# Kernel optimization log

Hardware: AMD Instinct MI355X
Metric: run time of the kernel (lower is better)

## Reference

```python
import jax, jax.numpy as jnp
import numpy as np

B, F, L, T, U, A, CF = 512, 80, 111, 222, 20, 10, 32  # batch, feat, enc_len, dec_steps, lstm units, attn units, conv filters


def setup_inputs() -> dict:
    key = jax.random.key(0)
    ks = jax.random.split(key, 16)
    g = lambda i, shape: jax.random.normal(ks[i], shape, jnp.float32) * 0.2
    return {
        "inputs": jax.random.normal(ks[0], (B, L, F), jnp.float32),
        "enc_Wx": g(1, (F, 4 * U)), "enc_Wh": g(2, (U, 4 * U)), "enc_b": jnp.zeros((4 * U,), jnp.float32),
        "att_Wq": g(3, (U, A)), "att_bq": jnp.zeros((A,), jnp.float32),
        "att_Wm": g(4, (U, A)), "att_bm": jnp.zeros((A,), jnp.float32),
        "att_V": g(5, (A, 1)), "att_bv": jnp.zeros((1,), jnp.float32),
        "loc_Wconv": g(6, (1, CF)),  # Conv1D kernel_size=1, no bias -> matmul
        "loc_Wd": g(7, (CF, A)),
        "dec_Wx": g(8, (U, 4 * U)), "dec_Wh": g(9, (U, 4 * U)), "dec_b": jnp.zeros((4 * U,), jnp.float32),
        "out_W": g(10, (U, 1)), "out_b": jnp.zeros((1,), jnp.float32),
    }


def _lstm(z, h, c):
    # Keras LSTMCell gate order: i, f, g(cell), o
    i, f, g, o = jnp.split(z, 4, axis=-1)
    c_new = jax.nn.sigmoid(f) * c + jax.nn.sigmoid(i) * jnp.tanh(g)
    h_new = jax.nn.sigmoid(o) * jnpp_tanh(c_new) if False else jax.nn.sigmoid(o) * jnp.tanh(c_new)
    return h_new, c_new


def reference(inputs, enc_Wx, enc_Wh, enc_b, att_Wq, att_bq, att_Wm, att_bm,
              att_V, att_bv, loc_Wconv, loc_Wd, dec_Wx, dec_Wh, dec_b, out_W, out_b):
    Bb, Ll = inputs.shape[0], inputs.shape[1]
    h0 = jnp.zeros((Bb, U), inputs.dtype)
    c0 = jnp.zeros((Bb, U), inputs.dtype)

    # ---- encoder LSTM(20), return_sequences ----
    def enc_step(carry, x_t):
        h, c = carry
        h, c = _lstm(x_t @ enc_Wx + h @ enc_Wh + enc_b, h, c)
        return (h, c), h
    _, enc_seq = jax.lax.scan(enc_step, (h0, c0), jnp.swapaxes(inputs, 0, 1))
    enc_out = jnp.swapaxes(enc_seq, 0, 1)                 # [B, L, U]
    mem_proj = enc_out @ att_Wm + att_bm                  # hoisted memory projection [B, L, A]

    # ---- decoder: location-sensitive attention + LSTMCell per step ----
    def dec_step(carry, _):
        h, c, prev_attn = carry                           # prev_attn: [B, L, 1]
        # Source unpacks Keras states as (c, h) but Keras order is [h, c]:
        # the query is actually the LSTM cell state. Replicated faithfully.
        q = c @ att_Wq + att_bq                           # [B, A]
        loc = jnp.tanh((prev_attn @ loc_Wconv) @ loc_Wd)  # kernel_size=1 conv == matmul, [B, L, A]
        score = jnp.tanh(mem_proj + q[:, None, :] + loc) @ att_V + att_bv  # [B, L, 1]
        attn = jax.nn.softmax(score, axis=1)              # softmax over encoder length
        ctx = jnp.sum(attn * enc_out, axis=1)             # [B, U]
        h_new, c_new = _lstm(ctx @ dec_Wx + h @ dec_Wh + dec_b, h, c)
        y = jnp.tanh(h_new @ out_W + out_b)               # [B, 1]
        return (h_new, c_new, attn), y

    a0 = jnp.zeros((Bb, Ll, 1), inputs.dtype)
    _, ys = jax.lax.scan(dec_step, (h0, c0, a0), None, length=T)
    return jnp.swapaxes(ys, 0, 1)                         # [B, T, 1] == output[:, :, :-length]
```

## Files before the change

kernel.cpp:

```cpp
#include <hip/hip_runtime.h>
#include <math.h>

#define NB    512
#define FDIM  80
#define LEN   111
#define TDEC  222
#define CFDIM 32
#define EOS   113

typedef float v2 __attribute__((ext_vector_type(2)));

__device__ __forceinline__ float rcpf(float x){ return __builtin_amdgcn_rcpf(x); }
__device__ __forceinline__ float sigm(float x){ return rcpf(1.0f + __expf(-x)); }
__device__ __forceinline__ float ftanh(float x){
  float e = __expf(2.0f*x);
  return 1.0f - 2.0f*rcpf(e + 1.0f);
}

template<int CTRL, int ROW_MASK>
__device__ __forceinline__ float dpp_add(float x){
  int yi = __builtin_amdgcn_update_dpp(0, __builtin_bit_cast(int, x), CTRL, ROW_MASK, 0xf, false);
  return x + __builtin_bit_cast(float, yi);
}
__device__ __forceinline__ float wave_sum(float x){
  x = dpp_add<0x111, 0xf>(x);
  x = dpp_add<0x112, 0xf>(x);
  x = dpp_add<0x114, 0xf>(x);
  x = dpp_add<0x118, 0xf>(x);
  x = dpp_add<0x142, 0xa>(x);
  x = dpp_add<0x143, 0xc>(x);
  return __builtin_bit_cast(float, __builtin_amdgcn_readlane(__builtin_bit_cast(int, x), 63));
}
#define RL(x, u) __builtin_bit_cast(float, __builtin_amdgcn_readlane(__builtin_bit_cast(int, (x)), (u)))

__global__ __launch_bounds__(64, 1)
void attn_rnn_kernel(const float* __restrict__ g_in,
                     const float* __restrict__ enc_Wx, const float* __restrict__ enc_Wh, const float* __restrict__ enc_b,
                     const float* __restrict__ att_Wq, const float* __restrict__ att_bq,
                     const float* __restrict__ att_Wm, const float* __restrict__ att_bm,
                     const float* __restrict__ att_V,  const float* __restrict__ att_bv,
                     const float* __restrict__ loc_Wc, const float* __restrict__ loc_Wd,
                     const float* __restrict__ dec_Wx, const float* __restrict__ dec_Wh, const float* __restrict__ dec_b,
                     const float* __restrict__ out_W,  const float* __restrict__ out_b,
                     float* __restrict__ g_out)
{
  __shared__ float xp[LEN*80];
  __shared__ float eoT[20*EOS];
  __shared__ float Wm_s[200];

  const int lane = threadIdx.x;
  const int b    = blockIdx.x;
  const float* inp = g_in + (size_t)b * LEN * FDIM;

  for (int k = lane; k < 200; k += 64) Wm_s[k] = att_Wm[k];

  float V[10], wloc[10], bmv[10];
  #pragma unroll
  for (int a = 0; a < 10; a++){ V[a] = att_V[a]; bmv[a] = att_bm[a]; wloc[a] = 0.f; }
  for (int cf = 0; cf < CFDIM; ++cf){
    float lwc = loc_Wc[cf];
    #pragma unroll
    for (int a = 0; a < 10; a++) wloc[a] += lwc * loc_Wd[cf*10 + a];
  }
  const float bv = att_bv[0];
  const float ob = out_b[0];
  const float bq_l = att_bq[(lane < 10) ? lane : 0];
  const float outw = (lane < 20) ? out_W[lane] : 0.f;
  float SB = bv;
  #pragma unroll
  for (int a = 0; a < 10; a++) SB += V[a];

  {
    float wxc[80];
    #pragma unroll
    for (int i = 0; i < 80; i++) wxc[i] = enc_Wx[i*80 + lane];
    const float ebj = enc_b[lane];
    for (int t = 0; t < LEN; t++){
      const float* xr = inp + t*FDIM;
      float a0=0.f,a1=0.f,a2=0.f,a3=0.f;
      #pragma unroll
      for (int i = 0; i < 80; i += 4){
        a0 += xr[i  ]*wxc[i  ]; a1 += xr[i+1]*wxc[i+1];
        a2 += xr[i+2]*wxc[i+2]; a3 += xr[i+3]*wxc[i+3];
      }
      xp[t*80 + lane] = ebj + ((a0+a1)+(a2+a3));
    }
  }
  {
    const int col = 64 + (lane >> 2);
    float wxc[80];
    #pragma unroll
    for (int i = 0; i < 80; i++) wxc[i] = enc_Wx[i*80 + col];
    const float ebj = enc_b[col];
    for (int t = (lane & 3); t < LEN; t += 4){
      const float* xr = inp + t*FDIM;
      float a0=0.f,a1=0.f,a2=0.f,a3=0.f;
      #pragma unroll
      for (int i = 0; i < 80; i += 4){
        a0 += xr[i  ]*wxc[i  ]; a1 += xr[i+1]*wxc[i+1];
        a2 += xr[i+2]*wxc[i+2]; a3 += xr[i+3]*wxc[i+3];
      }
      xp[t*80 + col] = ebj + ((a0+a1)+(a2+a3));
    }
  }

  const int ur = lane & 31;
  const int u0 = (ur < 20) ? ur : 0;
  const int cA = (lane >= 32) ? (u0 + 40) : u0;
  const int cB = cA + 20;
  v2 whp[20];
  #pragma unroll
  for (int u = 0; u < 20; u++)
    whp[u] = (v2){ enc_Wh[u*80 + cA], enc_Wh[u*80 + cB] };
  __syncthreads();

  float s_h[20];
  #pragma unroll
  for (int u = 0; u < 20; u++) s_h[u] = 0.f;
  float c_enc = 0.f;
  for (int t = 0; t < LEN; t++){
    v2 ac0 = (v2){ xp[t*80 + cA], xp[t*80 + cB] };
    v2 ac1 = (v2){0.f,0.f}, ac2 = (v2){0.f,0.f}, ac3 = (v2){0.f,0.f};
    #pragma unroll
    for (int u = 0; u < 20; u += 4){
      ac0 += s_h[u  ]*whp[u  ];
      ac1 += s_h[u+1]*whp[u+1];
      ac2 += s_h[u+2]*whp[u+2];
      ac3 += s_h[u+3]*whp[u+3];
    }
    v2 zp = (ac0 + ac1) + (ac2 + ac3);
    float ox = __shfl_xor(zp.x, 32, 64);
    float oy = __shfl_xor(zp.y, 32, 64);
    float hval = 0.f;
    if (lane < 20){
      c_enc = sigm(zp.y)*c_enc + sigm(zp.x)*ftanh(ox);
      hval  = sigm(oy)*ftanh(c_enc);
      eoT[lane*EOS + t] = hval;
    }
    #pragma unroll
    for (int u = 0; u < 20; u++) s_h[u] = RL(hval, u);
  }
  __syncthreads();

  const int l1 = (lane < 47) ? lane + 64 : lane;
  float er0[20], er1[20];
  #pragma unroll
  for (int u = 0; u < 20; u++){ er0[u] = eoT[u*EOS + lane]; er1[u] = eoT[u*EOS + l1]; }
  float mp0[10], mp1[10];
  #pragma unroll
  for (int a = 0; a < 10; a++){
    float m0 = bmv[a], m1 = bmv[a];
    #pragma unroll
    for (int u = 0; u < 20; u++){ m0 += er0[u]*Wm_s[u*10 + a]; m1 += er1[u]*Wm_s[u*10 + a]; }
    mp0[a] = m0; mp1[a] = m1;
  }

  v2 dwxp[20], dwhp[20];
  #pragma unroll
  for (int u = 0; u < 20; u++){
    dwxp[u] = (v2){ dec_Wx[u*80 + cA], dec_Wx[u*80 + cB] };
    dwhp[u] = (v2){ dec_Wh[u*80 + cA], dec_Wh[u*80 + cB] };
  }
  const v2 dbp = (v2){ dec_b[cA], dec_b[cB] };
  float wq[20];
  if (lane < 10){
    #pragma unroll
    for (int u = 0; u < 20; u++) wq[u] = att_Wq[u*10 + lane];
  }

  float s_c[20];
  #pragma unroll
  for (int u = 0; u < 20; u++){ s_c[u] = 0.f; s_h[u] = 0.f; }

  float ap0 = 0.f, ap1 = 0.f, c_dec = 0.f;
  for (int t = 0; t < TDEC; t++){
    float qv = bq_l;
    if (lane < 10){
      float qa = 0.f, qb = 0.f;
      #pragma unroll
      for (int u = 0; u < 20; u += 2){ qa += s_c[u]*wq[u]; qb += s_c[u+1]*wq[u+1]; }
      qv += qa + qb;
    }
    float s_q[10];
    #pragma unroll
    for (int a = 0; a < 10; a++) s_q[a] = RL(qv, a);

    float r00 = 0.f, r01 = 0.f, r10 = 0.f, r11 = 0.f;
    #pragma unroll
    for (int a = 0; a < 10; a += 2){
      float pre0 = mp0[a]   + s_q[a]   + ftanh(wloc[a]*ap0);
      float pre1 = mp1[a]   + s_q[a]   + ftanh(wloc[a]*ap1);
      float pr20 = mp0[a+1] + s_q[a+1] + ftanh(wloc[a+1]*ap0);
      float pr21 = mp1[a+1] + s_q[a+1] + ftanh(wloc[a+1]*ap1);
      r00 += V[a]  *rcpf(__expf(2.0f*pre0) + 1.0f);
      r01 += V[a]  *rcpf(__expf(2.0f*pre1) + 1.0f);
      r10 += V[a+1]*rcpf(__expf(2.0f*pr20) + 1.0f);
      r11 += V[a+1]*rcpf(__expf(2.0f*pr21) + 1.0f);
    }
    float e0 = __expf(SB - 2.0f*(r00 + r10));
    float e1 = (lane < 47) ? __expf(SB - 2.0f*(r01 + r11)) : 0.f;
    float inv = rcpf(wave_sum(e0 + e1));
    ap0 = e0*inv; ap1 = e1*inv;

    float ws[20];
    #pragma unroll
    for (int u = 0; u < 20; u++) ws[u] = wave_sum(e0*er0[u] + e1*er1[u]);

    v2 zx0 = (v2){0.f,0.f}, zx1 = (v2){0.f,0.f};
    v2 zh0 = dbp,            zh1 = (v2){0.f,0.f};
    #pragma unroll
    for (int u = 0; u < 20; u += 2){
      zx0 += ws[u]   *dwxp[u];
      zx1 += ws[u+1] *dwxp[u+1];
      zh0 += s_h[u]  *dwhp[u];
      zh1 += s_h[u+1]*dwhp[u+1];
    }
    v2 zzh = zh0 + zh1;
    v2 zzx = zx0 + zx1;
    v2 zp;
    zp.x = zzh.x + zzx.x*inv;
    zp.y = zzh.y + zzx.y*inv;
    float ox = __shfl_xor(zp.x, 32, 64);
    float oy = __shfl_xor(zp.y, 32, 64);

    float hval = 0.f;
    if (lane < 20){
      c_dec = sigm(zp.y)*c_dec + sigm(zp.x)*ftanh(ox);
      hval  = sigm(oy)*ftanh(c_dec);
    }

    #pragma unroll
    for (int u = 0; u < 20; u++){ s_c[u] = RL(c_dec, u); s_h[u] = RL(hval, u); }

    float pv = wave_sum(hval*outw);
    if (lane == 0) g_out[(size_t)b*TDEC + t] = ftanh(pv + ob);
  }
}

extern "C" void kernel_launch(void* const* d_in, const int* in_sizes, int n_in,
                              void* d_out, int out_size, void* d_ws, size_t ws_size,
                              hipStream_t stream) {
  const float* g_in   = (const float*)d_in[0];
  const float* enc_Wx = (const float*)d_in[1];
  const float* enc_Wh = (const float*)d_in[2];
  const float* enc_b  = (const float*)d_in[3];
  const float* att_Wq = (const float*)d_in[4];
  const float* att_bq = (const float*)d_in[5];
  const float* att_Wm = (const float*)d_in[6];
  const float* att_bm = (const float*)d_in[7];
  const float* att_V  = (const float*)d_in[8];
  const float* att_bv = (const float*)d_in[9];
  const float* loc_Wc = (const float*)d_in[10];
  const float* loc_Wd = (const float*)d_in[11];
  const float* dec_Wx = (const float*)d_in[12];
  const float* dec_Wh = (const float*)d_in[13];
  const float* dec_b  = (const float*)d_in[14];
  const float* out_W  = (const float*)d_in[15];
  const float* out_b  = (const float*)d_in[16];
  float* g_out = (float*)d_out;

  hipLaunchKernelGGL(attn_rnn_kernel, dim3(NB), dim3(64), 0, stream,
                     g_in, enc_Wx, enc_Wh, enc_b, att_Wq, att_bq, att_Wm, att_bm,
                     att_V, att_bv, loc_Wc, loc_Wd, dec_Wx, dec_Wh, dec_b,
                     out_W, out_b, g_out);
}
```

Measured before the change: 568.9 us.

## Process two batch elements per wavefront to interleave independent recurrences

Each 64-lane block now handles two batch rows and runs their encoder and decoder recurrences interleaved in the same instruction stream. The goal is to hide the latency of the serial dependency chains (wave reductions, readlanes, transcendental ops) by giving the scheduler two independent chains to overlap. To fit two batch rows in shared memory, the encoder input projection is computed in two halves of the sequence. This roughly doubles register pressure, which risks spills, and halves the grid to 256 blocks, which lowers CU occupancy.

```diff
diff --git a/kernel.cpp b/kernel.cpp
--- a/kernel.cpp
+++ b/kernel.cpp
@@ -1,12 +1,13 @@
 #include <hip/hip_runtime.h>
 #include <math.h>
 
-#define NB    512
+#define NB    256
 #define FDIM  80
 #define LEN   111
 #define TDEC  222
 #define CFDIM 32
 #define EOS   113
+#define HLF   56
 
 typedef float v2 __attribute__((ext_vector_type(2)));
 
@@ -44,13 +45,14 @@
                      const float* __restrict__ out_W,  const float* __restrict__ out_b,
                      float* __restrict__ g_out)
 {
-  __shared__ float xp[LEN*80];
-  __shared__ float eoT[20*EOS];
+  __shared__ float xpA[HLF*80], xpB[HLF*80];
+  __shared__ float eoTA[20*EOS], eoTB[20*EOS];
   __shared__ float Wm_s[200];
 
   const int lane = threadIdx.x;
-  const int b    = blockIdx.x;
-  const float* inp = g_in + (size_t)b * LEN * FDIM;
+  const int bA   = 2*blockIdx.x, bB = bA + 1;
+  const float* inpA = g_in + (size_t)bA * LEN * FDIM;
+  const float* inpB = g_in + (size_t)bB * LEN * FDIM;
 
   for (int k = lane; k < 200; k += 64) Wm_s[k] = att_Wm[k];
 
@@ -70,40 +72,6 @@
   #pragma unroll
   for (int a = 0; a < 10; a++) SB += V[a];
 
-  {
-    float wxc[80];
-    #pragma unroll
-    for (int i = 0; i < 80; i++) wxc[i] = enc_Wx[i*80 + lane];
-    const float ebj = enc_b[lane];
-    for (int t = 0; t < LEN; t++){
-      const float* xr = inp + t*FDIM;
-      float a0=0.f,a1=0.f,a2=0.f,a3=0.f;
-      #pragma unroll
-      for (int i = 0; i < 80; i += 4){
-        a0 += xr[i  ]*wxc[i  ]; a1 += xr[i+1]*wxc[i+1];
-        a2 += xr[i+2]*wxc[i+2]; a3 += xr[i+3]*wxc[i+3];
-      }
-      xp[t*80 + lane] = ebj + ((a0+a1)+(a2+a3));
-    }
-  }
-  {
-    const int col = 64 + (lane >> 2);
-    float wxc[80];
-    #pragma unroll
-    for (int i = 0; i < 80; i++) wxc[i] = enc_Wx[i*80 + col];
-    const float ebj = enc_b[col];
-    for (int t = (lane & 3); t < LEN; t += 4){
-      const float* xr = inp + t*FDIM;
-      float a0=0.f,a1=0.f,a2=0.f,a3=0.f;
-      #pragma unroll
-      for (int i = 0; i < 80; i += 4){
-        a0 += xr[i  ]*wxc[i  ]; a1 += xr[i+1]*wxc[i+1];
-        a2 += xr[i+2]*wxc[i+2]; a3 += xr[i+3]*wxc[i+3];
-      }
-      xp[t*80 + col] = ebj + ((a0+a1)+(a2+a3));
-    }
-  }
-
   const int ur = lane & 31;
   const int u0 = (ur < 20) ? ur : 0;
   const int cA = (lane >= 32) ? (u0 + 40) : u0;
@@ -112,47 +80,110 @@
   #pragma unroll
   for (int u = 0; u < 20; u++)
     whp[u] = (v2){ enc_Wh[u*80 + cA], enc_Wh[u*80 + cB] };
+
+  float s_hA[20], s_hB[20];
+  #pragma unroll
+  for (int u = 0; u < 20; u++){ s_hA[u] = 0.f; s_hB[u] = 0.f; }
+  float c_encA = 0.f, c_encB = 0.f;
+
+  for (int half = 0; half < 2; ++half){
+    const int t0 = half*HLF;
+    const int tn = half ? (LEN - HLF) : HLF;
+    __syncthreads();
+    {
+      float wxc[80];
+      #pragma unroll
+      for (int i = 0; i < 80; i++) wxc[i] = enc_Wx[i*80 + lane];
+      const float ebj = enc_b[lane];
+      for (int tt = 0; tt < tn; tt++){
+        const float* xrA = inpA + (t0+tt)*FDIM;
+        const float* xrB = inpB + (t0+tt)*FDIM;
+        float pA0=0.f,pA1=0.f,pA2=0.f,pA3=0.f;
+        float pB0=0.f,pB1=0.f,pB2=0.f,pB3=0.f;
+        #pragma unroll
+        for (int i = 0; i < 80; i += 4){
+          pA0 += xrA[i  ]*wxc[i  ]; pA1 += xrA[i+1]*wxc[i+1];
+          pA2 += xrA[i+2]*wxc[i+2]; pA3 += xrA[i+3]*wxc[i+3];
+          pB0 += xrB[i  ]*wxc[i  ]; pB1 += xrB[i+1]*wxc[i+1];
+          pB2 += xrB[i+2]*wxc[i+2]; pB3 += xrB[i+3]*wxc[i+3];
+        }
+        xpA[tt*80 + lane] = ebj + ((pA0+pA1)+(pA2+pA3));
+        xpB[tt*80 + lane] = ebj + ((pB0+pB1)+(pB2+pB3));
+      }
+    }
+    {
+      const int col = 64 + (lane >> 2);
+      float wxc[80];
+      #pragma unroll
+      for (int i = 0; i < 80; i++) wxc[i] = enc_Wx[i*80 + col];
+      const float ebj = enc_b[col];
+      for (int tt = (lane & 3); tt < tn; tt += 4){
+        const float* xrA = inpA + (t0+tt)*FDIM;
+        const float* xrB = inpB + (t0+tt)*FDIM;
+        float pA0=0.f,pA1=0.f,pA2=0.f,pA3=0.f;
+        float pB0=0.f,pB1=0.f,pB2=0.f,pB3=0.f;
+        #pragma unroll
+        for (int i = 0; i < 80; i += 4){
+          pA0 += xrA[i  ]*wxc[i  ]; pA1 += xrA[i+1]*wxc[i+1];
+          pA2 += xrA[i+2]*wxc[i+2]; pA3 += xrA[i+3]*wxc[i+3];
+          pB0 += xrB[i  ]*wxc[i  ]; pB1 += xrB[i+1]*wxc[i+1];
+          pB2 += xrB[i+2]*wxc[i+2]; pB3 += xrB[i+3]*wxc[i+3];
+        }
+        xpA[tt*80 + col] = ebj + ((pA0+pA1)+(pA2+pA3));
+        xpB[tt*80 + col] = ebj + ((pB0+pB1)+(pB2+pB3));
+      }
+    }
+    __syncthreads();
+    for (int tt = 0; tt < tn; tt++){
+      const int t = t0 + tt;
+      v2 aA0 = (v2){ xpA[tt*80 + cA], xpA[tt*80 + cB] };
+      v2 aB0 = (v2){ xpB[tt*80 + cA], xpB[tt*80 + cB] };
+      v2 aA1 = (v2){0.f,0.f}, aA2 = (v2){0.f,0.f}, aA3 = (v2){0.f,0.f};
+      v2 aB1 = (v2){0.f,0.f}, aB2 = (v2){0.f,0.f}, aB3 = (v2){0.f,0.f};
+      #pragma unroll
+      for (int u = 0; u < 20; u += 4){
+        aA0 += s_hA[u  ]*whp[u  ]; aB0 += s_hB[u  ]*whp[u  ];
+        aA1 += s_hA[u+1]*whp[u+1]; aB1 += s_hB[u+1]*whp[u+1];
+        aA2 += s_hA[u+2]*whp[u+2]; aB2 += s_hB[u+2]*whp[u+2];
+        aA3 += s_hA[u+3]*whp[u+3]; aB3 += s_hB[u+3]*whp[u+3];
+      }
+      v2 zA = (aA0 + aA1) + (aA2 + aA3);
+      v2 zB = (aB0 + aB1) + (aB2 + aB3);
+      float oxA = __shfl_xor(zA.x, 32, 64), oyA = __shfl_xor(zA.y, 32, 64);
+      float oxB = __shfl_xor(zB.x, 32, 64), oyB = __shfl_xor(zB.y, 32, 64);
+      float hA = 0.f, hB = 0.f;
+      if (lane < 20){
+        c_encA = sigm(zA.y)*c_encA + sigm(zA.x)*ftanh(oxA);
+        hA     = sigm(oyA)*ftanh(c_encA);
+        eoTA[lane*EOS + t] = hA;
+        c_encB = sigm(zB.y)*c_encB + sigm(zB.x)*ftanh(oxB);
+        hB     = sigm(oyB)*ftanh(c_encB);
+        eoTB[lane*EOS + t] = hB;
+      }
+      #pragma unroll
+      for (int u = 0; u < 20; u++){ s_hA[u] = RL(hA, u); s_hB[u] = RL(hB, u); }
+    }
+  }
   __syncthreads();
 
-  float s_h[20];
-  #pragma unroll
-  for (int u = 0; u < 20; u++) s_h[u] = 0.f;
-  float c_enc = 0.f;
-  for (int t = 0; t < LEN; t++){
-    v2 ac0 = (v2){ xp[t*80 + cA], xp[t*80 + cB] };
-    v2 ac1 = (v2){0.f,0.f}, ac2 = (v2){0.f,0.f}, ac3 = (v2){0.f,0.f};
-    #pragma unroll
-    for (int u = 0; u < 20; u += 4){
-      ac0 += s_h[u  ]*whp[u  ];
-      ac1 += s_h[u+1]*whp[u+1];
-      ac2 += s_h[u+2]*whp[u+2];
-      ac3 += s_h[u+3]*whp[u+3];
-    }
-    v2 zp = (ac0 + ac1) + (ac2 + ac3);
-    float ox = __shfl_xor(zp.x, 32, 64);
-    float oy = __shfl_xor(zp.y, 32, 64);
-    float hval = 0.f;
-    if (lane < 20){
-      c_enc = sigm(zp.y)*c_enc + sigm(zp.x)*ftanh(ox);
-      hval  = sigm(oy)*ftanh(c_enc);
-      eoT[lane*EOS + t] = hval;
-    }
-    #pragma unroll
-    for (int u = 0; u < 20; u++) s_h[u] = RL(hval, u);
-  }
-  __syncthreads();
-
   const int l1 = (lane < 47) ? lane + 64 : lane;
-  float er0[20], er1[20];
-  #pragma unroll
-  for (int u = 0; u < 20; u++){ er0[u] = eoT[u*EOS + lane]; er1[u] = eoT[u*EOS + l1]; }
-  float mp0[10], mp1[10];
+  float erA0[20], erA1[20], erB0[20], erB1[20];
+  #pragma unroll
+  for (int u = 0; u < 20; u++){
+    erA0[u] = eoTA[u*EOS + lane]; erA1[u] = eoTA[u*EOS + l1];
+    erB0[u] = eoTB[u*EOS + lane]; erB1[u] = eoTB[u*EOS + l1];
+  }
+  float mpA0[10], mpA1[10], mpB0[10], mpB1[10];
   #pragma unroll
   for (int a = 0; a < 10; a++){
-    float m0 = bmv[a], m1 = bmv[a];
-    #pragma unroll
-    for (int u = 0; u < 20; u++){ m0 += er0[u]*Wm_s[u*10 + a]; m1 += er1[u]*Wm_s[u*10 + a]; }
-    mp0[a] = m0; mp1[a] = m1;
+    float mA0 = bmv[a], mA1 = bmv[a], mB0 = bmv[a], mB1 = bmv[a];
+    #pragma unroll
+    for (int u = 0; u < 20; u++){
+      float w = Wm_s[u*10 + a];
+      mA0 += erA0[u]*w; mA1 += erA1[u]*w;
+      mB0 += erB0[u]*w; mB1 += erB1[u]*w;
+    }
+    mpA0[a] = mA0; mpA1[a] = mA1; mpB0[a] = mB0; mpB1[a] = mB1;
   }
 
   v2 dwxp[20], dwhp[20];
@@ -168,72 +199,102 @@
     for (int u = 0; u < 20; u++) wq[u] = att_Wq[u*10 + lane];
   }
 
-  float s_c[20];
-  #pragma unroll
-  for (int u = 0; u < 20; u++){ s_c[u] = 0.f; s_h[u] = 0.f; }
-
-  float ap0 = 0.f, ap1 = 0.f, c_dec = 0.f;
+  float s_cA[20], s_cB[20];
+  #pragma unroll
+  for (int u = 0; u < 20; u++){ s_cA[u] = 0.f; s_cB[u] = 0.f; s_hA[u] = 0.f; s_hB[u] = 0.f; }
+
+  float apA0 = 0.f, apA1 = 0.f, apB0 = 0.f, apB1 = 0.f;
+  float c_decA = 0.f, c_decB = 0.f;
   for (int t = 0; t < TDEC; t++){
-    float qv = bq_l;
+    float qvA = bq_l, qvB = bq_l;
     if (lane < 10){
-      float qa = 0.f, qb = 0.f;
-      #pragma unroll
-      for (int u = 0; u < 20; u += 2){ qa += s_c[u]*wq[u]; qb += s_c[u+1]*wq[u+1]; }
-      qv += qa + qb;
-    }
-    float s_q[10];
-    #pragma unroll
-    for (int a = 0; a < 10; a++) s_q[a] = RL(qv, a);
-
-    float r00 = 0.f, r01 = 0.f, r10 = 0.f, r11 = 0.f;
+      float qa = 0.f, qb = 0.f, qc = 0.f, qd = 0.f;
+      #pragma unroll
+      for (int u = 0; u < 20; u += 2){
+        qa += s_cA[u]*wq[u]; qb += s_cA[u+1]*wq[u+1];
+        qc += s_cB[u]*wq[u]; qd += s_cB[u+1]*wq[u+1];
+      }
+      qvA += qa + qb; qvB += qc + qd;
+    }
+    float s_qA[10], s_qB[10];
+    #pragma unroll
+    for (int a = 0; a < 10; a++){ s_qA[a] = RL(qvA, a); s_qB[a] = RL(qvB, a); }
+
+    float rA00=0.f, rA01=0.f, rA10=0.f, rA11=0.f;
+    float rB00=0.f, rB01=0.f, rB10=0.f, rB11=0.f;
     #pragma unroll
     for (int a = 0; a < 10; a += 2){
-      float pre0 = mp0[a]   + s_q[a]   + ftanh(wloc[a]*ap0);
-      float pre1 = mp1[a]   + s_q[a]   + ftanh(wloc[a]*ap1);
-      float pr20 = mp0[a+1] + s_q[a+1] + ftanh(wloc[a+1]*ap0);
-      float pr21 = mp1[a+1] + s_q[a+1] + ftanh(wloc[a+1]*ap1);
-      r00 += V[a]  *rcpf(__expf(2.0f*pre0) + 1.0f);
-      r01 += V[a]  *rcpf(__expf(2.0f*pre1) + 1.0f);
-      r10 += V[a+1]*rcpf(__expf(2.0f*pr20) + 1.0f);
-      r11 += V[a+1]*rcpf(__expf(2.0f*pr21) + 1.0f);
-    }
-    float e0 = __expf(SB - 2.0f*(r00 + r10));
-    float e1 = (lane < 47) ? __expf(SB - 2.0f*(r01 + r11)) : 0.f;
-    float inv = rcpf(wave_sum(e0 + e1));
-    ap0 = e0*inv; ap1 = e1*inv;
-
-    float ws[20];
-    #pragma unroll
-    for (int u = 0; u < 20; u++) ws[u] = wave_sum(e0*er0[u] + e1*er1[u]);
-
-    v2 zx0 = (v2){0.f,0.f}, zx1 = (v2){0.f,0.f};
-    v2 zh0 = dbp,            zh1 = (v2){0.f,0.f};
+      float pA0 = mpA0[a]   + s_qA[a]   + ftanh(wloc[a]*apA0);
+      float pA1 = mpA1[a]   + s_qA[a]   + ftanh(wloc[a]*apA1);
+      float pA2 = mpA0[a+1] + s_qA[a+1] + ftanh(wloc[a+1]*apA0);
+      float pA3 = mpA1[a+1] + s_qA[a+1] + ftanh(wloc[a+1]*apA1);
+      float pB0 = mpB0[a]   + s_qB[a]   + ftanh(wloc[a]*apB0);
+      float pB1 = mpB1[a]   + s_qB[a]   + ftanh(wloc[a]*apB1);
+      float pB2 = mpB0[a+1] + s_qB[a+1] + ftanh(wloc[a+1]*apB0);
+      float pB3 = mpB1[a+1] + s_qB[a+1] + ftanh(wloc[a+1]*apB1);
+      rA00 += V[a]  *rcpf(__expf(2.0f*pA0) + 1.0f);
+      rA01 += V[a]  *rcpf(__expf(2.0f*pA1) + 1.0f);
+      rA10 += V[a+1]*rcpf(__expf(2.0f*pA2) + 1.0f);
+      rA11 += V[a+1]*rcpf(__expf(2.0f*pA3) + 1.0f);
+      rB00 += V[a]  *rcpf(__expf(2.0f*pB0) + 1.0f);
+      rB01 += V[a]  *rcpf(__expf(2.0f*pB1) + 1.0f);
+      rB10 += V[a+1]*rcpf(__expf(2.0f*pB2) + 1.0f);
+      rB11 += V[a+1]*rcpf(__expf(2.0f*pB3) + 1.0f);
+    }
+    float eA0 = __expf(SB - 2.0f*(rA00 + rA10));
+    float eA1 = (lane < 47) ? __expf(SB - 2.0f*(rA01 + rA11)) : 0.f;
+    float eB0 = __expf(SB - 2.0f*(rB00 + rB10));
+    float eB1 = (lane < 47) ? __expf(SB - 2.0f*(rB01 + rB11)) : 0.f;
+    float invA = rcpf(wave_sum(eA0 + eA1));
+    float invB = rcpf(wave_sum(eB0 + eB1));
+    apA0 = eA0*invA; apA1 = eA1*invA;
+    apB0 = eB0*invB; apB1 = eB1*invB;
+
+    v2 zxA0 = (v2){0.f,0.f}, zxA1 = (v2){0.f,0.f};
+    v2 zxB0 = (v2){0.f,0.f}, zxB1 = (v2){0.f,0.f};
+    v2 zhA0 = dbp, zhA1 = (v2){0.f,0.f};
+    v2 zhB0 = dbp, zhB1 = (v2){0.f,0.f};
     #pragma unroll
     for (int u = 0; u < 20; u += 2){
-      zx0 += ws[u]   *dwxp[u];
-      zx1 += ws[u+1] *dwxp[u+1];
-      zh0 += s_h[u]  *dwhp[u];
-      zh1 += s_h[u+1]*dwhp[u+1];
-    }
-    v2 zzh = zh0 + zh1;
-    v2 zzx = zx0 + zx1;
-    v2 zp;
-    zp.x = zzh.x + zzx.x*inv;
-    zp.y = zzh.y + zzx.y*inv;
-    float ox = __shfl_xor(zp.x, 32, 64);
-    float oy = __shfl_xor(zp.y, 32, 64);
-
-    float hval = 0.f;
+      float wA0 = wave_sum(eA0*erA0[u]   + eA1*erA1[u]);
+      float wB0 = wave_sum(eB0*erB0[u]   + eB1*erB1[u]);
+      float wA1 = wave_sum(eA0*erA0[u+1] + eA1*erA1[u+1]);
+      float wB1 = wave_sum(eB0*erB0[u+1] + eB1*erB1[u+1]);
+      zxA0 += wA0*dwxp[u]; zxA1 += wA1*dwxp[u+1];
+      zxB0 += wB0*dwxp[u]; zxB1 += wB1*dwxp[u+1];
+      zhA0 += s_hA[u]*dwhp[u]; zhA1 += s_hA[u+1]*dwhp[u+1];
+      zhB0 += s_hB[u]*dwhp[u]; zhB1 += s_hB[u+1]*dwhp[u+1];
+    }
+    v2 zA, zB;
+    {
+      v2 hA2 = zhA0 + zhA1, xA2 = zxA0 + zxA1;
+      v2 hB2 = zhB0 + zhB1, xB2 = zxB0 + zxB1;
+      zA.x = hA2.x + xA2.x*invA; zA.y = hA2.y + xA2.y*invA;
+      zB.x = hB2.x + xB2.x*invB; zB.y = hB2.y + xB2.y*invB;
+    }
+    float oxA = __shfl_xor(zA.x, 32, 64), oyA = __shfl_xor(zA.y, 32, 64);
+    float oxB = __shfl_xor(zB.x, 32, 64), oyB = __shfl_xor(zB.y, 32, 64);
+
+    float hA = 0.f, hB = 0.f;
     if (lane < 20){
-      c_dec = sigm(zp.y)*c_dec + sigm(zp.x)*ftanh(ox);
-      hval  = sigm(oy)*ftanh(c_dec);
-    }
-
-    #pragma unroll
-    for (int u = 0; u < 20; u++){ s_c[u] = RL(c_dec, u); s_h[u] = RL(hval, u); }
-
-    float pv = wave_sum(hval*outw);
-    if (lane == 0) g_out[(size_t)b*TDEC + t] = ftanh(pv + ob);
+      c_decA = sigm(zA.y)*c_decA + sigm(zA.x)*ftanh(oxA);
+      hA     = sigm(oyA)*ftanh(c_decA);
+      c_decB = sigm(zB.y)*c_decB + sigm(zB.x)*ftanh(oxB);
+      hB     = sigm(oyB)*ftanh(c_decB);
+    }
+
+    #pragma unroll
+    for (int u = 0; u < 20; u++){
+      s_cA[u] = RL(c_decA, u); s_hA[u] = RL(hA, u);
+      s_cB[u] = RL(c_decB, u); s_hB[u] = RL(hB, u);
+    }
+
+    float pvA = wave_sum(hA*outw);
+    float pvB = wave_sum(hB*outw);
+    if (lane == 0){
+      g_out[(size_t)bA*TDEC + t] = ftanh(pvA + ob);
+      g_out[(size_t)bB*TDEC + t] = ftanh(pvB + ob);
+    }
   }
 }
 
```

Result: slower. 1.160 ms (+103.8%).
